# Kernel tuning notes

Hardware: AMD Instinct MI355X
Metric: run time of the kernel (lower is better)

## Reference

```python
import jax, jax.numpy as jnp
import numpy as np

N_NODES = 50000
N_EDGES = 500000
IN_DIM = 128
HIDDEN = 32
HEADS = 8
OUT_DIM = HIDDEN * HEADS  # 256
NEG_SLOPE = 0.2


def setup_inputs() -> dict:
    key = jax.random.key(0)
    ks = jax.random.split(key, 10)
    s = lambda fan: 1.0 / np.sqrt(fan)
    x = jax.random.normal(ks[0], (N_NODES, IN_DIM), dtype=jnp.float32)
    edge_index = jax.random.randint(ks[1], (2, N_EDGES), 0, N_NODES, dtype=jnp.int32)
    W1 = jax.random.normal(ks[2], (IN_DIM, HEADS * HIDDEN), jnp.float32) * s(IN_DIM)
    a_src1 = jax.random.normal(ks[3], (HEADS, HIDDEN), jnp.float32) * s(HIDDEN)
    a_dst1 = jax.random.normal(ks[4], (HEADS, HIDDEN), jnp.float32) * s(HIDDEN)
    b1 = jnp.zeros((HEADS * HIDDEN,), jnp.float32)
    W2 = jax.random.normal(ks[5], (OUT_DIM, OUT_DIM), jnp.float32) * s(OUT_DIM)
    a_src2 = jax.random.normal(ks[6], (1, OUT_DIM), jnp.float32) * s(OUT_DIM)
    a_dst2 = jax.random.normal(ks[7], (1, OUT_DIM), jnp.float32) * s(OUT_DIM)
    b2 = jnp.zeros((OUT_DIM,), jnp.float32)
    return {"x": x, "edge_index": edge_index, "W1": W1, "a_src1": a_src1,
            "a_dst1": a_dst1, "b1": b1, "W2": W2, "a_src2": a_src2,
            "a_dst2": a_dst2, "b2": b2}


def _gat_layer(x, src, dst, W, a_src, a_dst, b, heads, ch, concat):
    N = x.shape[0]
    h = (x @ W).reshape(N, heads, ch)                      # [N,H,C]
    e_src = jnp.sum(h * a_src[None], axis=-1)              # [N,H]
    e_dst = jnp.sum(h * a_dst[None], axis=-1)              # [N,H]
    e = jax.nn.leaky_relu(e_src[src] + e_dst[dst], NEG_SLOPE)  # [E,H]
    # softmax over incoming edges of each destination node
    m = jax.ops.segment_max(e, dst, num_segments=N)        # [N,H]
    e = jnp.exp(e - m[dst])
    denom = jax.ops.segment_sum(e, dst, num_segments=N)    # [N,H]
    alpha = e / (denom[dst] + 1e-16)                       # [E,H]
    msg = h[src] * alpha[:, :, None]                       # [E,H,C]
    out = jax.ops.segment_sum(msg, dst, num_segments=N)    # [N,H,C]
    out = out.reshape(N, heads * ch) if concat else out.mean(axis=1)
    return out + b


def reference(x, edge_index, W1, a_src1, a_dst1, b1, W2, a_src2, a_dst2, b2):
    N = x.shape[0]
    # add self loops (PyG GATConv default)
    loops = jnp.arange(N, dtype=edge_index.dtype)
    src = jnp.concatenate([edge_index[0], loops])
    dst = jnp.concatenate([edge_index[1], loops])
    # dropout is identity in eval mode
    h = _gat_layer(x, src, dst, W1, a_src1, a_dst1, b1, HEADS, HIDDEN, True)
    h = jax.nn.elu(h)
    out = _gat_layer(h, src, dst, W2, a_src2, a_dst2, b2, 1, OUT_DIM, False)
    return out
```

## Files before the change

kernel.cpp:

```cpp
#include <hip/hip_runtime.h>
#include <math.h>

#define N_NODES 50000
#define E_ORIG  500000
#define E_TOT   550000
#define NB      196

typedef _Float16 half8 __attribute__((ext_vector_type(8)));
typedef _Float16 half4 __attribute__((ext_vector_type(4)));
typedef float    v4f   __attribute__((ext_vector_type(4)));

__global__ void k_zero(int* __restrict__ p, int n) {
    int i = blockIdx.x * blockDim.x + threadIdx.x;
    if (i < n) p[i] = 0;
}

__global__ void k_count(const int* __restrict__ ei, int* __restrict__ deg) {
    int e = blockIdx.x * blockDim.x + threadIdx.x;
    if (e >= E_TOT) return;
    int d = (e < E_ORIG) ? ei[E_ORIG + e] : (e - E_ORIG);
    atomicAdd(&deg[d], 1);
}

__global__ __launch_bounds__(256) void k_blocksum(const int* __restrict__ deg,
                                                  int* __restrict__ bsum) {
    int t = threadIdx.x;
    int i = blockIdx.x * 256 + t;
    int v = (i < N_NODES) ? deg[i] : 0;
#pragma unroll
    for (int mk = 1; mk < 64; mk <<= 1) v += __shfl_xor(v, mk, 64);
    __shared__ int ws[4];
    if ((t & 63) == 0) ws[t >> 6] = v;
    __syncthreads();
    if (t == 0) bsum[blockIdx.x] = ws[0] + ws[1] + ws[2] + ws[3];
}

__global__ __launch_bounds__(256) void k_scanbsum(const int* __restrict__ bsum,
                                                  int* __restrict__ boff) {
    __shared__ int s[256];
    int t = threadIdx.x;
    int v = (t < NB) ? bsum[t] : 0;
    s[t] = v;
    __syncthreads();
    for (int o = 1; o < 256; o <<= 1) {
        int x = (t >= o) ? s[t - o] : 0;
        __syncthreads();
        s[t] += x;
        __syncthreads();
    }
    if (t <= NB) boff[t] = (t == 0) ? 0 : s[t - 1];
}

__global__ __launch_bounds__(256) void k_offsets(const int* __restrict__ deg,
                                                 const int* __restrict__ boff,
                                                 int* __restrict__ offsets,
                                                 int* __restrict__ cur) {
    __shared__ int s[256];
    int t = threadIdx.x;
    int i = blockIdx.x * 256 + t;
    int v = (i < N_NODES) ? deg[i] : 0;
    s[t] = v;
    __syncthreads();
    for (int o = 1; o < 256; o <<= 1) {
        int x = (t >= o) ? s[t - o] : 0;
        __syncthreads();
        s[t] += x;
        __syncthreads();
    }
    int off = boff[blockIdx.x] + s[t] - v;
    if (i <= N_NODES) {
        offsets[i] = off;
        if (i < N_NODES) cur[i] = off;
    }
}

__global__ void k_scatter(const int* __restrict__ ei, int* __restrict__ cur,
                          int* __restrict__ csr_src) {
    int e = blockIdx.x * blockDim.x + threadIdx.x;
    if (e >= E_TOT) return;
    int s, d;
    if (e < E_ORIG) { s = ei[e]; d = ei[E_ORIG + e]; }
    else            { s = e - E_ORIG; d = s; }
    int slot = atomicAdd(&cur[d], 1);
    csr_src[slot] = s;
}

__global__ void k_prepw(const float* __restrict__ W1, const float* __restrict__ W2,
                        const float* __restrict__ as2, const float* __restrict__ ad2,
                        _Float16* __restrict__ w1t, _Float16* __restrict__ w2t,
                        float* __restrict__ vs2, float* __restrict__ vd2) {
    int i = blockIdx.x * blockDim.x + threadIdx.x;
    if (i < 128 * 256) {
        int k = i >> 8, c = i & 255;
        w1t[(size_t)c * 128 + k] = (_Float16)W1[i];
        return;
    }
    int j = i - 128 * 256;
    if (j < 256 * 256) {
        int k = j >> 8, c = j & 255;
        w2t[(size_t)c * 256 + k] = (_Float16)W2[j];
        return;
    }
    int k = j - 256 * 256;
    if (k < 256) {
        float s = 0.f, d = 0.f;
        for (int c = 0; c < 256; c++) {
            float w = W2[(size_t)k * 256 + c];
            s += w * as2[c];
            d += w * ad2[c];
        }
        vs2[k] = s;
        vd2[k] = d;
    }
}

__global__ __launch_bounds__(256) void k_gemm1(
    const float* __restrict__ X, const _Float16* __restrict__ Bt,
    const float* __restrict__ a_s, const float* __restrict__ a_d,
    _Float16* __restrict__ H, float* __restrict__ es, float* __restrict__ ed) {
    int t = threadIdx.x, w = t >> 6, lane = t & 63;
    int quad = lane >> 4, l16 = lane & 15;
    int row0 = blockIdx.x * 32;
    int colbase = w * 64;

    v4f acc[2][4];
#pragma unroll
    for (int i = 0; i < 2; i++)
#pragma unroll
        for (int j = 0; j < 4; j++) acc[i][j] = (v4f){0.f, 0.f, 0.f, 0.f};

    int r0 = row0 + l16;      if (r0 >= N_NODES) r0 = N_NODES - 1;
    int r1 = row0 + 16 + l16; if (r1 >= N_NODES) r1 = N_NODES - 1;
    const float4* a0p = (const float4*)(X + (size_t)r0 * 128) + quad * 2;
    const float4* a1p = (const float4*)(X + (size_t)r1 * 128) + quad * 2;
    const half8* bp[4];
#pragma unroll
    for (int ct = 0; ct < 4; ct++)
        bp[ct] = (const half8*)(Bt + (size_t)(colbase + ct * 16 + l16) * 128 + quad * 8);

#pragma unroll
    for (int kc = 0; kc < 4; kc++) {
        float4 f0 = a0p[kc * 8], f1 = a0p[kc * 8 + 1];
        float4 f2 = a1p[kc * 8], f3 = a1p[kc * 8 + 1];
        half8 av0 = (half8){(_Float16)f0.x, (_Float16)f0.y, (_Float16)f0.z, (_Float16)f0.w,
                            (_Float16)f1.x, (_Float16)f1.y, (_Float16)f1.z, (_Float16)f1.w};
        half8 av1 = (half8){(_Float16)f2.x, (_Float16)f2.y, (_Float16)f2.z, (_Float16)f2.w,
                            (_Float16)f3.x, (_Float16)f3.y, (_Float16)f3.z, (_Float16)f3.w};
#pragma unroll
        for (int ct = 0; ct < 4; ct++) {
            half8 bv = bp[ct][kc * 4];
            acc[0][ct] = __builtin_amdgcn_mfma_f32_16x16x32_f16(av0, bv, acc[0][ct], 0, 0, 0);
            acc[1][ct] = __builtin_amdgcn_mfma_f32_16x16x32_f16(av1, bv, acc[1][ct], 0, 0, 0);
        }
    }

    float asv[4], adv[4];
#pragma unroll
    for (int ct = 0; ct < 4; ct++) {
        asv[ct] = a_s[colbase + ct * 16 + l16];
        adv[ct] = a_d[colbase + ct * 16 + l16];
    }
#pragma unroll
    for (int rt = 0; rt < 2; rt++) {
#pragma unroll
        for (int hp = 0; hp < 2; hp++) {
#pragma unroll
            for (int reg = 0; reg < 4; reg++) {
                float ps = acc[rt][2 * hp][reg] * asv[2 * hp] +
                           acc[rt][2 * hp + 1][reg] * asv[2 * hp + 1];
                float pd = acc[rt][2 * hp][reg] * adv[2 * hp] +
                           acc[rt][2 * hp + 1][reg] * adv[2 * hp + 1];
#pragma unroll
                for (int mk = 1; mk < 16; mk <<= 1) {
                    ps += __shfl_xor(ps, mk, 64);
                    pd += __shfl_xor(pd, mk, 64);
                }
                if (l16 == 0) {
                    int row = row0 + rt * 16 + quad * 4 + reg;
                    if (row < N_NODES) {
                        int head = w * 2 + hp;
                        es[(size_t)row * 8 + head] = ps;
                        ed[(size_t)row * 8 + head] = pd;
                    }
                }
            }
        }
    }

    __shared__ _Float16 SH[32][264];
#pragma unroll
    for (int rt = 0; rt < 2; rt++)
#pragma unroll
        for (int ct = 0; ct < 4; ct++)
#pragma unroll
            for (int reg = 0; reg < 4; reg++)
                SH[rt * 16 + quad * 4 + reg][colbase + ct * 16 + l16] =
                    (_Float16)acc[rt][ct][reg];
    __syncthreads();
#pragma unroll
    for (int j = 0; j < 4; j++) {
        int c = j * 256 + t;
        int row = c >> 5, col8 = c & 31;
        int gr = row0 + row;
        if (gr < N_NODES)
            *(half8*)(H + (size_t)gr * 256 + col8 * 8) = *(const half8*)&SH[row][col8 * 8];
    }
}

__global__ __launch_bounds__(256) void k_gemm2(
    const _Float16* __restrict__ A, const _Float16* __restrict__ Bt,
    const float* __restrict__ bias, float* __restrict__ OUT) {
    int t = threadIdx.x, w = t >> 6, lane = t & 63;
    int quad = lane >> 4, l16 = lane & 15;
    int row0 = blockIdx.x * 32;
    int colbase = w * 64;

    v4f acc[2][4];
#pragma unroll
    for (int i = 0; i < 2; i++)
#pragma unroll
        for (int j = 0; j < 4; j++) acc[i][j] = (v4f){0.f, 0.f, 0.f, 0.f};

    int r0 = row0 + l16;      if (r0 >= N_NODES) r0 = N_NODES - 1;
    int r1 = row0 + 16 + l16; if (r1 >= N_NODES) r1 = N_NODES - 1;
    const half8* a0 = (const half8*)(A + (size_t)r0 * 256 + quad * 8);
    const half8* a1 = (const half8*)(A + (size_t)r1 * 256 + quad * 8);
    const half8* bp[4];
#pragma unroll
    for (int ct = 0; ct < 4; ct++)
        bp[ct] = (const half8*)(Bt + (size_t)(colbase + ct * 16 + l16) * 256 + quad * 8);

#pragma unroll
    for (int kc = 0; kc < 8; kc++) {
        half8 av0 = a0[kc * 4];
        half8 av1 = a1[kc * 4];
#pragma unroll
        for (int ct = 0; ct < 4; ct++) {
            half8 bv = bp[ct][kc * 4];
            acc[0][ct] = __builtin_amdgcn_mfma_f32_16x16x32_f16(av0, bv, acc[0][ct], 0, 0, 0);
            acc[1][ct] = __builtin_amdgcn_mfma_f32_16x16x32_f16(av1, bv, acc[1][ct], 0, 0, 0);
        }
    }

    __shared__ float SF[32][260];
#pragma unroll
    for (int rt = 0; rt < 2; rt++)
#pragma unroll
        for (int ct = 0; ct < 4; ct++)
#pragma unroll
            for (int reg = 0; reg < 4; reg++)
                SF[rt * 16 + quad * 4 + reg][colbase + ct * 16 + l16] = acc[rt][ct][reg];
    __syncthreads();
#pragma unroll
    for (int j = 0; j < 8; j++) {
        int c = j * 256 + t;
        int row = c >> 6, c4 = c & 63;
        int gr = row0 + row;
        if (gr < N_NODES) {
            float4 v = *(const float4*)&SF[row][c4 * 4];
            float4 bb = ((const float4*)bias)[c4];
            float4 o = make_float4(v.x + bb.x, v.y + bb.y, v.z + bb.z, v.w + bb.w);
            *(float4*)(OUT + (size_t)gr * 256 + c4 * 4) = o;
        }
    }
}

__global__ __launch_bounds__(256) void k_agg1(
    const _Float16* __restrict__ H1, const float* __restrict__ es,
    const float* __restrict__ ed, const int* __restrict__ offsets,
    const int* __restrict__ csr_src, const float* __restrict__ b1,
    const float* __restrict__ vs2, const float* __restrict__ vd2,
    _Float16* __restrict__ out1, float* __restrict__ es2,
    float* __restrict__ ed2) {
    int t = threadIdx.x, w = t >> 6, lane = t & 63;
    int n = blockIdx.x * 4 + w;
    int hB = lane >> 3;
    int beg = offsets[n];
    int deg = offsets[n + 1] - beg;
    float edl = ed[(size_t)n * 8 + hB];

    const half4* __restrict__ Hl = (const half4*)H1 + lane;
    float a0 = 0.f, a1 = 0.f, a2 = 0.f, a3 = 0.f, den = 0.f;

    for (int base = 0; base < deg; base += 64) {
        int rem = deg - base; if (rem > 64) rem = 64;
        int idx = beg + base + lane;
        if (idx >= E_TOT) idx = E_TOT - 1;
        int sreg = csr_src[idx];
        int i = 0;
        for (; i + 1 < rem; i += 2) {
            int s0 = __shfl(sreg, i);
            int s1 = __shfl(sreg, i + 1);
            float l0 = es[(size_t)s0 * 8 + hB] + edl;
            float l1 = es[(size_t)s1 * 8 + hB] + edl;
            l0 = l0 > 0.f ? l0 : 0.2f * l0;
            l1 = l1 > 0.f ? l1 : 0.2f * l1;
            float w0 = __expf(l0), w1 = __expf(l1);
            half4 h0 = Hl[(size_t)s0 * 64];
            half4 h1 = Hl[(size_t)s1 * 64];
            a0 += w0 * (float)h0[0]; a1 += w0 * (float)h0[1];
            a2 += w0 * (float)h0[2]; a3 += w0 * (float)h0[3];
            a0 += w1 * (float)h1[0]; a1 += w1 * (float)h1[1];
            a2 += w1 * (float)h1[2]; a3 += w1 * (float)h1[3];
            den += w0 + w1;
        }
        if (i < rem) {
            int s0 = __shfl(sreg, i);
            float l0 = es[(size_t)s0 * 8 + hB] + edl;
            l0 = l0 > 0.f ? l0 : 0.2f * l0;
            float w0 = __expf(l0);
            half4 h0 = Hl[(size_t)s0 * 64];
            a0 += w0 * (float)h0[0]; a1 += w0 * (float)h0[1];
            a2 += w0 * (float)h0[2]; a3 += w0 * (float)h0[3];
            den += w0;
        }
    }

    float r = 1.f / (den + 1e-16f);
    float4 bb = ((const float4*)b1)[lane];
    float o0 = a0 * r + bb.x, o1 = a1 * r + bb.y;
    float o2 = a2 * r + bb.z, o3 = a3 * r + bb.w;
    o0 = o0 > 0.f ? o0 : __expf(o0) - 1.f;
    o1 = o1 > 0.f ? o1 : __expf(o1) - 1.f;
    o2 = o2 > 0.f ? o2 : __expf(o2) - 1.f;
    o3 = o3 > 0.f ? o3 : __expf(o3) - 1.f;
    ((half4*)(out1 + (size_t)n * 256))[lane] =
        (half4){(_Float16)o0, (_Float16)o1, (_Float16)o2, (_Float16)o3};

    float4 vs = ((const float4*)vs2)[lane];
    float4 vd = ((const float4*)vd2)[lane];
    float ps = o0 * vs.x + o1 * vs.y + o2 * vs.z + o3 * vs.w;
    float pd = o0 * vd.x + o1 * vd.y + o2 * vd.z + o3 * vd.w;
#pragma unroll
    for (int mk = 1; mk < 64; mk <<= 1) {
        ps += __shfl_xor(ps, mk, 64);
        pd += __shfl_xor(pd, mk, 64);
    }
    if (lane == 0) { es2[n] = ps; ed2[n] = pd; }
}

__global__ __launch_bounds__(256) void k_agg2(
    const _Float16* __restrict__ O1, const float* __restrict__ es2,
    const float* __restrict__ ed2, const int* __restrict__ offsets,
    const int* __restrict__ csr_src, _Float16* __restrict__ xagg) {
    int t = threadIdx.x, w = t >> 6, lane = t & 63;
    int n = blockIdx.x * 4 + w;
    int beg = offsets[n];
    int deg = offsets[n + 1] - beg;
    float edn = ed2[n];

    const half4* __restrict__ Ol = (const half4*)O1 + lane;
    float a0 = 0.f, a1 = 0.f, a2 = 0.f, a3 = 0.f, den = 0.f;

    for (int base = 0; base < deg; base += 64) {
        int rem = deg - base; if (rem > 64) rem = 64;
        int idx = beg + base + lane;
        if (idx >= E_TOT) idx = E_TOT - 1;
        int sreg = csr_src[idx];
        int i = 0;
        for (; i + 1 < rem; i += 2) {
            int s0 = __shfl(sreg, i);
            int s1 = __shfl(sreg, i + 1);
            float l0 = es2[s0] + edn;
            float l1 = es2[s1] + edn;
            l0 = l0 > 0.f ? l0 : 0.2f * l0;
            l1 = l1 > 0.f ? l1 : 0.2f * l1;
            float w0 = __expf(l0), w1 = __expf(l1);
            half4 h0 = Ol[(size_t)s0 * 64];
            half4 h1 = Ol[(size_t)s1 * 64];
            a0 += w0 * (float)h0[0]; a1 += w0 * (float)h0[1];
            a2 += w0 * (float)h0[2]; a3 += w0 * (float)h0[3];
            a0 += w1 * (float)h1[0]; a1 += w1 * (float)h1[1];
            a2 += w1 * (float)h1[2]; a3 += w1 * (float)h1[3];
            den += w0 + w1;
        }
        if (i < rem) {
            int s0 = __shfl(sreg, i);
            float l0 = es2[s0] + edn;
            l0 = l0 > 0.f ? l0 : 0.2f * l0;
            float w0 = __expf(l0);
            half4 h0 = Ol[(size_t)s0 * 64];
            a0 += w0 * (float)h0[0]; a1 += w0 * (float)h0[1];
            a2 += w0 * (float)h0[2]; a3 += w0 * (float)h0[3];
            den += w0;
        }
    }

    float r = 1.f / (den + 1e-16f);
    ((half4*)(xagg + (size_t)n * 256))[lane] =
        (half4){(_Float16)(a0 * r), (_Float16)(a1 * r),
                (_Float16)(a2 * r), (_Float16)(a3 * r)};
}

extern "C" void kernel_launch(void* const* d_in, const int* in_sizes, int n_in,
                              void* d_out, int out_size, void* d_ws, size_t ws_size,
                              hipStream_t stream) {
    const float* x   = (const float*)d_in[0];
    const int*   ei  = (const int*)d_in[1];
    const float* W1  = (const float*)d_in[2];
    const float* as1 = (const float*)d_in[3];
    const float* ad1 = (const float*)d_in[4];
    const float* b1  = (const float*)d_in[5];
    const float* W2  = (const float*)d_in[6];
    const float* as2 = (const float*)d_in[7];
    const float* ad2 = (const float*)d_in[8];
    const float* b2  = (const float*)d_in[9];
    float* out = (float*)d_out;

    char* ws = (char*)d_ws;
    size_t off = 0;
    auto alloc = [&](size_t bytes) {
        void* p = ws + off;
        off = (off + bytes + 255) & ~(size_t)255;
        return p;
    };
    _Float16* h1h     = (_Float16*)alloc((size_t)N_NODES * 256 * 2);
    _Float16* out1h   = (_Float16*)alloc((size_t)N_NODES * 256 * 2);
    _Float16* xagg    = (_Float16*)alloc((size_t)N_NODES * 256 * 2);
    _Float16* w1t     = (_Float16*)alloc((size_t)128 * 256 * 2);
    _Float16* w2t     = (_Float16*)alloc((size_t)256 * 256 * 2);
    float*    es1     = (float*)alloc((size_t)N_NODES * 8 * 4);
    float*    ed1     = (float*)alloc((size_t)N_NODES * 8 * 4);
    float*    es2     = (float*)alloc((size_t)N_NODES * 4);
    float*    ed2     = (float*)alloc((size_t)N_NODES * 4);
    float*    vs2     = (float*)alloc(256 * 4);
    float*    vd2     = (float*)alloc(256 * 4);
    int*      deg     = (int*)alloc((size_t)N_NODES * 4);
    int*      offsets = (int*)alloc((size_t)(N_NODES + 1) * 4);
    int*      cur     = (int*)alloc((size_t)N_NODES * 4);
    int*      csr_src = (int*)alloc((size_t)E_TOT * 4);
    int*      bsum    = (int*)alloc((size_t)NB * 4);
    int*      boff    = (int*)alloc((size_t)(NB + 1) * 4);

    const int TB = 256;
    int gridN = (N_NODES + TB - 1) / TB;
    int gridE = (E_TOT + TB - 1) / TB;
    int gridG = (N_NODES + 31) / 32;
    int gridA = N_NODES / 4;

    k_zero<<<gridN, TB, 0, stream>>>(deg, N_NODES);
    k_count<<<gridE, TB, 0, stream>>>(ei, deg);
    k_blocksum<<<NB, TB, 0, stream>>>(deg, bsum);
    k_scanbsum<<<1, TB, 0, stream>>>(bsum, boff);
    k_offsets<<<NB, TB, 0, stream>>>(deg, boff, offsets, cur);
    k_scatter<<<gridE, TB, 0, stream>>>(ei, cur, csr_src);

    int prepN = 128 * 256 + 256 * 256 + 256;
    k_prepw<<<(prepN + TB - 1) / TB, TB, 0, stream>>>(W1, W2, as2, ad2,
                                                      w1t, w2t, vs2, vd2);

    k_gemm1<<<gridG, TB, 0, stream>>>(x, w1t, as1, ad1, h1h, es1, ed1);
    k_agg1<<<gridA, TB, 0, stream>>>(h1h, es1, ed1, offsets, csr_src, b1,
                                     vs2, vd2, out1h, es2, ed2);

    k_agg2<<<gridA, TB, 0, stream>>>(out1h, es2, ed2, offsets, csr_src, xagg);
    k_gemm2<<<gridG, TB, 0, stream>>>(xagg, w2t, b2, out);
}
```

Before: 329.0 us.

## Precompute edge attention weights in separate kernels before aggregation

Adds k_wts1 and k_wts2, which compute exp(leaky_relu(es[src]+ed[dst])) per CSR edge, stored in edge order. The aggregation kernels then load these precomputed weights instead of gathering es and running exp inside the dependent gather loop. The scatter kernel now also writes csr_dst, and zeroing of deg is folded into k_prepw, which removes one launch. The cost is two extra launches plus writing and rereading about 18 MB of edge weights and 2 MB of csr_dst. Row addressing also switches to 32-bit shift arithmetic.

```diff
diff --git a/kernel.cpp b/kernel.cpp
--- a/kernel.cpp
+++ b/kernel.cpp
@@ -9,11 +9,6 @@
 typedef _Float16 half8 __attribute__((ext_vector_type(8)));
 typedef _Float16 half4 __attribute__((ext_vector_type(4)));
 typedef float    v4f   __attribute__((ext_vector_type(4)));
-
-__global__ void k_zero(int* __restrict__ p, int n) {
-    int i = blockIdx.x * blockDim.x + threadIdx.x;
-    if (i < n) p[i] = 0;
-}
 
 __global__ void k_count(const int* __restrict__ ei, int* __restrict__ deg) {
     int e = blockIdx.x * blockDim.x + threadIdx.x;
@@ -75,7 +70,7 @@
 }
 
 __global__ void k_scatter(const int* __restrict__ ei, int* __restrict__ cur,
-                          int* __restrict__ csr_src) {
+                          int* __restrict__ csr_src, int* __restrict__ csr_dst) {
     int e = blockIdx.x * blockDim.x + threadIdx.x;
     if (e >= E_TOT) return;
     int s, d;
@@ -83,12 +78,14 @@
     else            { s = e - E_ORIG; d = s; }
     int slot = atomicAdd(&cur[d], 1);
     csr_src[slot] = s;
+    csr_dst[slot] = d;
 }
 
 __global__ void k_prepw(const float* __restrict__ W1, const float* __restrict__ W2,
                         const float* __restrict__ as2, const float* __restrict__ ad2,
                         _Float16* __restrict__ w1t, _Float16* __restrict__ w2t,
-                        float* __restrict__ vs2, float* __restrict__ vd2) {
+                        float* __restrict__ vs2, float* __restrict__ vd2,
+                        int* __restrict__ deg) {
     int i = blockIdx.x * blockDim.x + threadIdx.x;
     if (i < 128 * 256) {
         int k = i >> 8, c = i & 255;
@@ -101,17 +98,44 @@
         w2t[(size_t)c * 256 + k] = (_Float16)W2[j];
         return;
     }
-    int k = j - 256 * 256;
-    if (k < 256) {
+    j -= 256 * 256;
+    if (j < 256) {
         float s = 0.f, d = 0.f;
         for (int c = 0; c < 256; c++) {
-            float w = W2[(size_t)k * 256 + c];
+            float w = W2[(size_t)j * 256 + c];
             s += w * as2[c];
             d += w * ad2[c];
         }
-        vs2[k] = s;
-        vd2[k] = d;
-    }
+        vs2[j] = s;
+        vd2[j] = d;
+        return;
+    }
+    j -= 256;
+    if (j < N_NODES) deg[j] = 0;
+}
+
+__global__ __launch_bounds__(256) void k_wts1(
+    const int* __restrict__ csr_src, const int* __restrict__ csr_dst,
+    const float* __restrict__ es, const float* __restrict__ ed,
+    float* __restrict__ w1w) {
+    int i = blockIdx.x * blockDim.x + threadIdx.x;
+    if (i >= E_TOT * 8) return;
+    int e = i >> 3, h = i & 7;
+    int s = csr_src[e], d = csr_dst[e];
+    float l = es[(size_t)s * 8 + h] + ed[(size_t)d * 8 + h];
+    l = l > 0.f ? l : 0.2f * l;
+    w1w[i] = __expf(l);
+}
+
+__global__ __launch_bounds__(256) void k_wts2(
+    const int* __restrict__ csr_src, const int* __restrict__ csr_dst,
+    const float* __restrict__ es2, const float* __restrict__ ed2,
+    float* __restrict__ w2w) {
+    int e = blockIdx.x * blockDim.x + threadIdx.x;
+    if (e >= E_TOT) return;
+    float l = es2[csr_src[e]] + ed2[csr_dst[e]];
+    l = l > 0.f ? l : 0.2f * l;
+    w2w[e] = __expf(l);
 }
 
 __global__ __launch_bounds__(256) void k_gemm1(
@@ -266,20 +290,19 @@
 }
 
 __global__ __launch_bounds__(256) void k_agg1(
-    const _Float16* __restrict__ H1, const float* __restrict__ es,
-    const float* __restrict__ ed, const int* __restrict__ offsets,
-    const int* __restrict__ csr_src, const float* __restrict__ b1,
-    const float* __restrict__ vs2, const float* __restrict__ vd2,
-    _Float16* __restrict__ out1, float* __restrict__ es2,
-    float* __restrict__ ed2) {
+    const _Float16* __restrict__ H1, const float* __restrict__ w1w,
+    const int* __restrict__ offsets, const int* __restrict__ csr_src,
+    const float* __restrict__ b1, const float* __restrict__ vs2,
+    const float* __restrict__ vd2, _Float16* __restrict__ out1,
+    float* __restrict__ es2, float* __restrict__ ed2) {
     int t = threadIdx.x, w = t >> 6, lane = t & 63;
     int n = blockIdx.x * 4 + w;
     int hB = lane >> 3;
     int beg = offsets[n];
     int deg = offsets[n + 1] - beg;
-    float edl = ed[(size_t)n * 8 + hB];
-
-    const half4* __restrict__ Hl = (const half4*)H1 + lane;
+
+    const char* __restrict__ Hb = (const char*)H1 + lane * 8;
+    const float* __restrict__ pw = w1w + (size_t)beg * 8 + hB;
     float a0 = 0.f, a1 = 0.f, a2 = 0.f, a3 = 0.f, den = 0.f;
 
     for (int base = 0; base < deg; base += 64) {
@@ -291,13 +314,10 @@
         for (; i + 1 < rem; i += 2) {
             int s0 = __shfl(sreg, i);
             int s1 = __shfl(sreg, i + 1);
-            float l0 = es[(size_t)s0 * 8 + hB] + edl;
-            float l1 = es[(size_t)s1 * 8 + hB] + edl;
-            l0 = l0 > 0.f ? l0 : 0.2f * l0;
-            l1 = l1 > 0.f ? l1 : 0.2f * l1;
-            float w0 = __expf(l0), w1 = __expf(l1);
-            half4 h0 = Hl[(size_t)s0 * 64];
-            half4 h1 = Hl[(size_t)s1 * 64];
+            float w0 = pw[(base + i) * 8];
+            float w1 = pw[(base + i + 1) * 8];
+            half4 h0 = *(const half4*)(Hb + ((unsigned)s0 << 9));
+            half4 h1 = *(const half4*)(Hb + ((unsigned)s1 << 9));
             a0 += w0 * (float)h0[0]; a1 += w0 * (float)h0[1];
             a2 += w0 * (float)h0[2]; a3 += w0 * (float)h0[3];
             a0 += w1 * (float)h1[0]; a1 += w1 * (float)h1[1];
@@ -306,10 +326,8 @@
         }
         if (i < rem) {
             int s0 = __shfl(sreg, i);
-            float l0 = es[(size_t)s0 * 8 + hB] + edl;
-            l0 = l0 > 0.f ? l0 : 0.2f * l0;
-            float w0 = __expf(l0);
-            half4 h0 = Hl[(size_t)s0 * 64];
+            float w0 = pw[(base + i) * 8];
+            half4 h0 = *(const half4*)(Hb + ((unsigned)s0 << 9));
             a0 += w0 * (float)h0[0]; a1 += w0 * (float)h0[1];
             a2 += w0 * (float)h0[2]; a3 += w0 * (float)h0[3];
             den += w0;
@@ -340,16 +358,15 @@
 }
 
 __global__ __launch_bounds__(256) void k_agg2(
-    const _Float16* __restrict__ O1, const float* __restrict__ es2,
-    const float* __restrict__ ed2, const int* __restrict__ offsets,
-    const int* __restrict__ csr_src, _Float16* __restrict__ xagg) {
+    const _Float16* __restrict__ O1, const float* __restrict__ w2w,
+    const int* __restrict__ offsets, const int* __restrict__ csr_src,
+    _Float16* __restrict__ xagg) {
     int t = threadIdx.x, w = t >> 6, lane = t & 63;
     int n = blockIdx.x * 4 + w;
     int beg = offsets[n];
     int deg = offsets[n + 1] - beg;
-    float edn = ed2[n];
-
-    const half4* __restrict__ Ol = (const half4*)O1 + lane;
+
+    const char* __restrict__ Ob = (const char*)O1 + lane * 8;
     float a0 = 0.f, a1 = 0.f, a2 = 0.f, a3 = 0.f, den = 0.f;
 
     for (int base = 0; base < deg; base += 64) {
@@ -357,17 +374,15 @@
         int idx = beg + base + lane;
         if (idx >= E_TOT) idx = E_TOT - 1;
         int sreg = csr_src[idx];
+        float wreg = w2w[idx];
         int i = 0;
         for (; i + 1 < rem; i += 2) {
             int s0 = __shfl(sreg, i);
             int s1 = __shfl(sreg, i + 1);
-            float l0 = es2[s0] + edn;
-            float l1 = es2[s1] + edn;
-            l0 = l0 > 0.f ? l0 : 0.2f * l0;
-            l1 = l1 > 0.f ? l1 : 0.2f * l1;
-            float w0 = __expf(l0), w1 = __expf(l1);
-            half4 h0 = Ol[(size_t)s0 * 64];
-            half4 h1 = Ol[(size_t)s1 * 64];
+            float w0 = __shfl(wreg, i);
+            float w1 = __shfl(wreg, i + 1);
+            half4 h0 = *(const half4*)(Ob + ((unsigned)s0 << 9));
+            half4 h1 = *(const half4*)(Ob + ((unsigned)s1 << 9));
             a0 += w0 * (float)h0[0]; a1 += w0 * (float)h0[1];
             a2 += w0 * (float)h0[2]; a3 += w0 * (float)h0[3];
             a0 += w1 * (float)h1[0]; a1 += w1 * (float)h1[1];
@@ -376,10 +391,8 @@
         }
         if (i < rem) {
             int s0 = __shfl(sreg, i);
-            float l0 = es2[s0] + edn;
-            l0 = l0 > 0.f ? l0 : 0.2f * l0;
-            float w0 = __expf(l0);
-            half4 h0 = Ol[(size_t)s0 * 64];
+            float w0 = __shfl(wreg, i);
+            half4 h0 = *(const half4*)(Ob + ((unsigned)s0 << 9));
             a0 += w0 * (float)h0[0]; a1 += w0 * (float)h0[1];
             a2 += w0 * (float)h0[2]; a3 += w0 * (float)h0[3];
             den += w0;
@@ -425,34 +438,37 @@
     float*    ed2     = (float*)alloc((size_t)N_NODES * 4);
     float*    vs2     = (float*)alloc(256 * 4);
     float*    vd2     = (float*)alloc(256 * 4);
+    float*    w1w     = (float*)alloc((size_t)E_TOT * 8 * 4);
+    float*    w2w     = (float*)alloc((size_t)E_TOT * 4);
     int*      deg     = (int*)alloc((size_t)N_NODES * 4);
     int*      offsets = (int*)alloc((size_t)(N_NODES + 1) * 4);
     int*      cur     = (int*)alloc((size_t)N_NODES * 4);
     int*      csr_src = (int*)alloc((size_t)E_TOT * 4);
+    int*      csr_dst = (int*)alloc((size_t)E_TOT * 4);
     int*      bsum    = (int*)alloc((size_t)NB * 4);
     int*      boff    = (int*)alloc((size_t)(NB + 1) * 4);
 
     const int TB = 256;
-    int gridN = (N_NODES + TB - 1) / TB;
     int gridE = (E_TOT + TB - 1) / TB;
     int gridG = (N_NODES + 31) / 32;
     int gridA = N_NODES / 4;
 
-    k_zero<<<gridN, TB, 0, stream>>>(deg, N_NODES);
+    int prepN = 128 * 256 + 256 * 256 + 256 + N_NODES;
+    k_prepw<<<(prepN + TB - 1) / TB, TB, 0, stream>>>(W1, W2, as2, ad2,
+                                                      w1t, w2t, vs2, vd2, deg);
     k_count<<<gridE, TB, 0, stream>>>(ei, deg);
     k_blocksum<<<NB, TB, 0, stream>>>(deg, bsum);
     k_scanbsum<<<1, TB, 0, stream>>>(bsum, boff);
     k_offsets<<<NB, TB, 0, stream>>>(deg, boff, offsets, cur);
-    k_scatter<<<gridE, TB, 0, stream>>>(ei, cur, csr_src);
-
-    int prepN = 128 * 256 + 256 * 256 + 256;
-    k_prepw<<<(prepN + TB - 1) / TB, TB, 0, stream>>>(W1, W2, as2, ad2,
-                                                      w1t, w2t, vs2, vd2);
+    k_scatter<<<gridE, TB, 0, stream>>>(ei, cur, csr_src, csr_dst);
 
     k_gemm1<<<gridG, TB, 0, stream>>>(x, w1t, as1, ad1, h1h, es1, ed1);
-    k_agg1<<<gridA, TB, 0, stream>>>(h1h, es1, ed1, offsets, csr_src, b1,
+    k_wts1<<<(E_TOT * 8 + TB - 1) / TB, TB, 0, stream>>>(csr_src, csr_dst,
+                                                         es1, ed1, w1w);
+    k_agg1<<<gridA, TB, 0, stream>>>(h1h, w1w, offsets, csr_src, b1,
                                      vs2, vd2, out1h, es2, ed2);
 
-    k_agg2<<<gridA, TB, 0, stream>>>(out1h, es2, ed2, offsets, csr_src, xagg);
+    k_wts2<<<gridE, TB, 0, stream>>>(csr_src, csr_dst, es2, ed2, w2w);
+    k_agg2<<<gridA, TB, 0, stream>>>(out1h, w2w, offsets, csr_src, xagg);
     k_gemm2<<<gridG, TB, 0, stream>>>(xagg, w2t, b2, out);
 }
```

New measurement: 339.4 us. 1.03x slower.
